# Kernel tuning notes

Measured on AMD Instinct MI355X. Metric: run time of the kernel, lower is better.

Reference implementation:

```python
import jax, jax.numpy as jnp
import numpy as np

B, L = 64, 2048
G, K, D = 16, 16, 256
N = G * K
STEPS = 32
MAX_NODES = 50
LN_EPS = 1e-5


def _gelu(x):
    return jax.nn.gelu(x, approximate=False)  # torch nn.GELU default = exact erf


def _mlp2(x, w1, b1, w2, b2):
    return _gelu(x @ w1 + b1) @ w2 + b2


def setup_inputs() -> dict:
    key = jax.random.key(0)
    ki = iter(jax.random.split(key, 64))
    def nrm(shape, s=0.02):
        return jax.random.normal(next(ki), shape, dtype=jnp.float32) * s
    inp = {}
    inp['src'] = jax.random.randint(next(ki), (B, L), 0, MAX_NODES)
    inp['rel'] = jax.random.randint(next(ki), (B, L), 0, 2)
    inp['tgt'] = jax.random.randint(next(ki), (B, L), 0, MAX_NODES)
    inp['mask'] = jnp.ones((B, L), dtype=bool)  # unused by forward, kept for signature parity
    inp['qsrc'] = jax.random.randint(next(ki), (B,), 0, MAX_NODES)
    inp['qtgt'] = jax.random.randint(next(ki), (B,), 0, MAX_NODES)
    inp['node_embed'] = nrm((MAX_NODES, D), 1.0)
    inp['rel_embed'] = nrm((2, D), 1.0)
    inp['edge_w1'] = nrm((3 * D, D)); inp['edge_b1'] = jnp.zeros((D,), jnp.float32)
    inp['edge_w2'] = nrm((D, D)); inp['edge_b2'] = jnp.zeros((D,), jnp.float32)
    inp['query_w1'] = nrm((2 * D, D)); inp['query_b1'] = jnp.zeros((D,), jnp.float32)
    inp['query_w2'] = nrm((D, D)); inp['query_b2'] = jnp.zeros((D,), jnp.float32)
    inp['gproj'] = nrm((D, G))
    inp['sproj'] = nrm((D, K))
    inp['msg_w1'] = nrm((D, 2 * D)); inp['msg_b1'] = jnp.zeros((2 * D,), jnp.float32)
    inp['msg_w2'] = nrm((2 * D, D)); inp['msg_b2'] = jnp.zeros((D,), jnp.float32)
    inp['gate_w1'] = nrm((D, D)); inp['gate_b1'] = jnp.zeros((D,), jnp.float32)
    inp['gate_w2'] = nrm((D, 1)); inp['gate_b2'] = jnp.zeros((1,), jnp.float32)
    inp['upd_w1'] = nrm((2 * D, 2 * D)); inp['upd_b1'] = jnp.zeros((2 * D,), jnp.float32)
    inp['upd_w2'] = nrm((2 * D, D)); inp['upd_b2'] = jnp.zeros((D,), jnp.float32)
    inp['ln_w'] = jnp.ones((D,), jnp.float32); inp['ln_b'] = jnp.zeros((D,), jnp.float32)
    inp['S_init'] = nrm((N, D))
    inp['head_w1'] = nrm((2 * D, D)); inp['head_b1'] = jnp.zeros((D,), jnp.float32)
    inp['head_w2'] = nrm((D, 2)); inp['head_b2'] = jnp.zeros((2,), jnp.float32)
    return inp


def _forward(src, rel, tgt, mask, qsrc, qtgt,
             node_embed, rel_embed,
             edge_w1, edge_b1, edge_w2, edge_b2,
             query_w1, query_b1, query_w2, query_b2,
             gproj, sproj,
             msg_w1, msg_b1, msg_w2, msg_b2,
             gate_w1, gate_b1, gate_w2, gate_b2,
             upd_w1, upd_b1, upd_w2, upd_b2,
             ln_w, ln_b, S_init,
             head_w1, head_b1, head_w2, head_b2):
    Bsz = src.shape[0]
    se = node_embed[jnp.clip(src, 0, MAX_NODES - 1)]          # (B, L, D)
    te = node_embed[jnp.clip(tgt, 0, MAX_NODES - 1)]
    re = rel_embed[rel]
    Xe = _mlp2(jnp.concatenate([se, re, te], -1), edge_w1, edge_b1, edge_w2, edge_b2)
    q = _mlp2(jnp.concatenate([node_embed[jnp.clip(qsrc, 0, MAX_NODES - 1)],
                               node_embed[jnp.clip(qtgt, 0, MAX_NODES - 1)]], -1),
              query_w1, query_b1, query_w2, query_b2)
    X = jnp.concatenate([Xe, q[:, None, :]], axis=1)          # (B, L+1, D)

    # Eval-mode hierarchical hard routing; X is constant across steps so the
    # message aggregation is loop-invariant and computed once (identical math).
    msg = _mlp2(X, msg_w1, msg_b1, msg_w2, msg_b2)
    gate = jax.nn.sigmoid(_mlp2(X, gate_w1, gate_b1, gate_w2, gate_b2))
    gated_msg = msg * gate                                    # (B, L+1, D)
    ga = jax.nn.one_hot(jnp.argmax(X @ gproj, axis=-1), G, dtype=X.dtype)  # (B,L+1,G)
    sa = jax.nn.one_hot(jnp.argmax(X @ sproj, axis=-1), K, dtype=X.dtype)  # (B,L+1,K)
    full_assign = (ga[..., :, None] * sa[..., None, :]).reshape(Bsz, X.shape[1], N)
    incoming = jnp.einsum('bln,bld->bnd', full_assign, gated_msg)          # (B, N, D)

    S0 = jnp.broadcast_to(S_init, (Bsz, N, D))

    def step(S, _):
        u = _mlp2(jnp.concatenate([S, incoming], -1), upd_w1, upd_b1, upd_w2, upd_b2)
        S = S + u
        mu = S.mean(-1, keepdims=True)
        var = ((S - mu) ** 2).mean(-1, keepdims=True)
        S = (S - mu) / jnp.sqrt(var + LN_EPS) * ln_w + ln_b
        return S, None

    S, _ = jax.lax.scan(step, S0, None, length=STEPS)
    bi = jnp.arange(Bsz)
    s_src = S[bi, jnp.clip(qsrc, 0, N - 1)]                   # (B, D)
    s_tgt = S[bi, jnp.clip(qtgt, 0, N - 1)]
    logits = _mlp2(jnp.concatenate([s_src, s_tgt], -1), head_w1, head_b1, head_w2, head_b2)
    return logits                                             # (B, 2)


def reference(src, rel, tgt, mask, qsrc, qtgt,
              node_embed, rel_embed,
              edge_w1, edge_b1, edge_w2, edge_b2,
              query_w1, query_b1, query_w2, query_b2,
              gproj, sproj,
              msg_w1, msg_b1, msg_w2, msg_b2,
              gate_w1, gate_b1, gate_w2, gate_b2,
              upd_w1, upd_b1, upd_w2, upd_b2,
              ln_w, ln_b, S_init,
              head_w1, head_b1, head_w2, head_b2):
    return _forward(src, rel, tgt, mask, qsrc, qtgt,
                    node_embed, rel_embed,
                    edge_w1, edge_b1, edge_w2, edge_b2,
                    query_w1, query_b1, query_w2, query_b2,
                    gproj, sproj,
                    msg_w1, msg_b1, msg_w2, msg_b2,
                    gate_w1, gate_b1, gate_w2, gate_b2,
                    upd_w1, upd_b1, upd_w2, upd_b2,
                    ln_w, ln_b, S_init,
                    head_w1, head_b1, head_w2, head_b2)
```

## Files before the change

### kernel.cpp

```cpp
#include <hip/hip_runtime.h>
#include <hip/hip_bf16.h>
#include <math.h>

#define NB     64
#define LL     2048
#define DD     256
#define NNODE  256
#define NSTEPS 32

typedef __hip_bfloat16 bf16;
typedef __attribute__((ext_vector_type(8))) short bf16x8;
typedef __attribute__((ext_vector_type(4))) float f32x4;

__device__ __forceinline__ float geluf(float x){ return 0.5f*x*(1.0f+erff(x*0.70710678118654752440f)); }
__device__ __forceinline__ short f2bs(float x){ bf16 h = __float2bfloat16(x); return __builtin_bit_cast(short, h); }
__device__ __forceinline__ float bs2f(short s){ bf16 h = __builtin_bit_cast(bf16, s); return __bfloat162float(h); }

__device__ __forceinline__ void split8(float4 a, float4 b, bf16x8& hi, bf16x8& lo){
  float av[8] = {a.x,a.y,a.z,a.w,b.x,b.y,b.z,b.w};
  #pragma unroll
  for(int j=0;j<8;j++){
    short h = f2bs(av[j]);
    hi[j] = h;
    lo[j] = f2bs(av[j] - bs2f(h));
  }
}
__device__ __forceinline__ bf16x8 cvt8(float4 a, float4 b){
  float av[8] = {a.x,a.y,a.z,a.w,b.x,b.y,b.z,b.w};
  bf16x8 v;
  #pragma unroll
  for(int j=0;j<8;j++) v[j] = f2bs(av[j]);
  return v;
}

__global__ __launch_bounds__(256) void k_precompute(const float* __restrict__ ne,
    const float* __restrict__ re, const float* __restrict__ ew1, const float* __restrict__ eb1,
    float* __restrict__ P){
  __shared__ float a[256];
  int row = blockIdx.x, j = threadIdx.x;
  const float* vec; const float* W;
  if(row < 50){ vec = ne + row*256; W = ew1; }
  else if(row < 52){ vec = re + (row-50)*256; W = ew1 + 256*256; }
  else { vec = ne + (row-52)*256; W = ew1 + 512*256; }
  a[j] = vec[j];
  __syncthreads();
  float acc = 0.f;
  for(int k=0;k<256;k++) acc += a[k]*W[k*256 + j];
  if(row >= 50 && row < 52) acc += eb1[j];
  P[row*256 + j] = acc;
}

__global__ __launch_bounds__(256) void k_query(const int* __restrict__ qsrc, const int* __restrict__ qtgt,
    const float* __restrict__ ne, const float* __restrict__ qw1, const float* __restrict__ qb1,
    const float* __restrict__ qw2, const float* __restrict__ qb2, float* __restrict__ qv){
  __shared__ float a[512];
  __shared__ float h[256];
  int b = blockIdx.x, j = threadIdx.x;
  int s = min(max(qsrc[b],0),49), t = min(max(qtgt[b],0),49);
  a[j]     = ne[s*256 + j];
  a[256+j] = ne[t*256 + j];
  __syncthreads();
  float acc = qb1[j];
  for(int k=0;k<512;k++) acc += a[k]*qw1[k*256+j];
  h[j] = geluf(acc);
  __syncthreads();
  float acc2 = qb2[j];
  for(int k=0;k<256;k++) acc2 += h[k]*qw2[k*256+j];
  qv[b*256+j] = acc2;
}

__global__ __launch_bounds__(256) void k_wprep(
    const float* __restrict__ uw1, const float* __restrict__ uw2,
    const float* __restrict__ ew2, const float* __restrict__ gw1,
    const float* __restrict__ mw1, const float* __restrict__ mw2,
    bf16* __restrict__ WTa, bf16* __restrict__ WT2,
    bf16* __restrict__ Weh, bf16* __restrict__ Wel, bf16* __restrict__ Wg,
    bf16* __restrict__ Wm1, bf16* __restrict__ Wm2){
  int i = blockIdx.x*256 + threadIdx.x;
  { int n = i >> 8, k = i & 255;  WTa[i] = __float2bfloat16(uw1[k*512 + n]); }
  { int n = i >> 9, k = i & 511;  WT2[i] = __float2bfloat16(uw2[k*256 + n]); }
  { int n = i >> 8, k = i & 255;  Wm1[i] = __float2bfloat16(mw1[k*512 + n]); }
  { int n = i >> 9, k = i & 511;  Wm2[i] = __float2bfloat16(mw2[k*256 + n]); }
  if(i < 65536){
    int n = i >> 8, k = i & 255;
    float v = ew2[k*256 + n];
    bf16 h = __float2bfloat16(v);
    Weh[i] = h;
    Wel[i] = __float2bfloat16(v - __bfloat162float(h));
    Wg[i]  = __float2bfloat16(gw1[k*256 + n]);
  }
}

#define AST 260
#define MST 520
__global__ __launch_bounds__(256,2) void k_edge_mfma(
    const int* __restrict__ src, const int* __restrict__ rel, const int* __restrict__ tgt,
    const float* __restrict__ P,
    const bf16* __restrict__ Weh, const bf16* __restrict__ Wel, const float* __restrict__ eb2,
    const bf16* __restrict__ Wg, const float* __restrict__ gb1,
    const float* __restrict__ gw2, const float* __restrict__ gb2,
    const float* __restrict__ gp, const float* __restrict__ sp,
    const bf16* __restrict__ Wm1, const float* __restrict__ mb1,
    const bf16* __restrict__ Wm2, const float* __restrict__ mb2,
    float* __restrict__ incoming)
{
  __shared__ __align__(16) float Af[32*AST];
  __shared__ __align__(16) float Xf[32*AST];
  __shared__ float pv[32*32];
  __shared__ float redG[32*4];
  __shared__ float gatev[32];
  __shared__ int   nidx[32];
  bf16* Mh = (bf16*)Af;

  int tid = threadIdx.x;
  int w = tid>>6, lane = tid&63, l15 = lane&15, l4 = lane>>4;
  int blk = blockIdx.x, b = blk>>6, r0 = (blk&63)*32;

  {
    int rr = tid&31, kb = (tid>>5)*32;
    int gr = b*LL + r0 + rr;
    int s = min(max(src[gr],0),49), rl = rel[gr]&1, t = min(max(tgt[gr],0),49);
    const float* ps = P + s*256;
    const float* pr = P + (50+rl)*256;
    const float* pt = P + (52+t)*256;
    #pragma unroll
    for(int j=0;j<32;j+=4){
      int k = kb+j;
      float4 vs = *(const float4*)(ps+k), vr = *(const float4*)(pr+k), vt = *(const float4*)(pt+k);
      float4 o;
      o.x = geluf(vs.x+vr.x+vt.x); o.y = geluf(vs.y+vr.y+vt.y);
      o.z = geluf(vs.z+vr.z+vt.z); o.w = geluf(vs.w+vr.w+vt.w);
      *(float4*)&Af[rr*AST + k] = o;
    }
  }
  __syncthreads();

  {
    f32x4 acc[2][4];
    #pragma unroll
    for(int mt=0;mt<2;mt++)
    #pragma unroll
    for(int nt=0;nt<4;nt++) acc[mt][nt] = (f32x4){0.f,0.f,0.f,0.f};
    for(int kc=0;kc<8;kc++){
      int k0 = kc*32 + l4*8;
      bf16x8 ah[2], al[2];
      #pragma unroll
      for(int mt=0;mt<2;mt++){
        const float* p = &Af[(mt*16+l15)*AST + k0];
        split8(*(const float4*)p, *(const float4*)(p+4), ah[mt], al[mt]);
      }
      #pragma unroll
      for(int nt=0;nt<4;nt++){
        int n = w*64 + nt*16 + l15;
        bf16x8 wh = *(const bf16x8*)&Weh[n*256 + k0];
        bf16x8 wl = *(const bf16x8*)&Wel[n*256 + k0];
        #pragma unroll
        for(int mt=0;mt<2;mt++){
          acc[mt][nt] = __builtin_amdgcn_mfma_f32_16x16x32_bf16(ah[mt], wh, acc[mt][nt], 0,0,0);
          acc[mt][nt] = __builtin_amdgcn_mfma_f32_16x16x32_bf16(ah[mt], wl, acc[mt][nt], 0,0,0);
          acc[mt][nt] = __builtin_amdgcn_mfma_f32_16x16x32_bf16(al[mt], wh, acc[mt][nt], 0,0,0);
        }
      }
    }
    #pragma unroll
    for(int nt=0;nt<4;nt++){
      int n = w*64 + nt*16 + l15;
      float bb = eb2[n];
      #pragma unroll
      for(int mt=0;mt<2;mt++)
      #pragma unroll
      for(int reg=0;reg<4;reg++){
        int r = mt*16 + l4*4 + reg;
        Xf[r*AST + n] = acc[mt][nt][reg] + bb;
      }
    }
  }
  __syncthreads();

  {
    f32x4 ag[2][4];
    #pragma unroll
    for(int mt=0;mt<2;mt++)
    #pragma unroll
    for(int nt=0;nt<4;nt++) ag[mt][nt] = (f32x4){0.f,0.f,0.f,0.f};
    for(int kc=0;kc<8;kc++){
      int k0 = kc*32 + l4*8;
      bf16x8 xa[2];
      #pragma unroll
      for(int mt=0;mt<2;mt++){
        const float* p = &Xf[(mt*16+l15)*AST + k0];
        xa[mt] = cvt8(*(const float4*)p, *(const float4*)(p+4));
      }
      #pragma unroll
      for(int nt=0;nt<4;nt++){
        int n = w*64 + nt*16 + l15;
        bf16x8 wv = *(const bf16x8*)&Wg[n*256 + k0];
        #pragma unroll
        for(int mt=0;mt<2;mt++)
          ag[mt][nt] = __builtin_amdgcn_mfma_f32_16x16x32_bf16(xa[mt], wv, ag[mt][nt], 0,0,0);
      }
    }
    float gpart[2][4] = {{0.f,0.f,0.f,0.f},{0.f,0.f,0.f,0.f}};
    #pragma unroll
    for(int nt=0;nt<4;nt++){
      int n = w*64 + nt*16 + l15;
      float gb = gb1[n], gw = gw2[n];
      #pragma unroll
      for(int mt=0;mt<2;mt++)
      #pragma unroll
      for(int reg=0;reg<4;reg++)
        gpart[mt][reg] += geluf(ag[mt][nt][reg] + gb)*gw;
    }
    #pragma unroll
    for(int mt=0;mt<2;mt++)
    #pragma unroll
    for(int reg=0;reg<4;reg++){
      float sv = gpart[mt][reg];
      #pragma unroll
      for(int o=1;o<16;o<<=1) sv += __shfl_xor(sv,o);
      if(l15==0) redG[(mt*16 + l4*4 + reg)*4 + w] = sv;
    }
  }
  {
    int r2 = tid>>3, g = tid&7, c0 = g*4;
    const float* W4 = (c0<16)? (gp + c0) : (sp + (c0-16));
    float4 p = {0.f,0.f,0.f,0.f};
    for(int k=0;k<256;k++){
      float x = Xf[r2*AST + k];
      float4 wv = *(const float4*)(W4 + k*16);
      p.x += x*wv.x; p.y += x*wv.y; p.z += x*wv.z; p.w += x*wv.w;
    }
    pv[r2*32+c0+0]=p.x; pv[r2*32+c0+1]=p.y; pv[r2*32+c0+2]=p.z; pv[r2*32+c0+3]=p.w;
  }
  __syncthreads();
  if(tid < 32){
    float ssum = redG[tid*4+0]+redG[tid*4+1]+redG[tid*4+2]+redG[tid*4+3] + gb2[0];
    gatev[tid] = 1.f/(1.f+expf(-ssum));
    float bg = pv[tid*32+0]; int big = 0;
    #pragma unroll
    for(int j=1;j<16;j++){ float x=pv[tid*32+j]; if(x>bg){bg=x;big=j;} }
    float bs = pv[tid*32+16]; int bis = 0;
    #pragma unroll
    for(int j=1;j<16;j++){ float x=pv[tid*32+16+j]; if(x>bs){bs=x;bis=j;} }
    nidx[tid] = big*16 + bis;
  }
  __syncthreads();

  {
    f32x4 a1[2][8];
    #pragma unroll
    for(int mt=0;mt<2;mt++)
    #pragma unroll
    for(int nt=0;nt<8;nt++) a1[mt][nt] = (f32x4){0.f,0.f,0.f,0.f};
    for(int kc=0;kc<8;kc++){
      int k0 = kc*32 + l4*8;
      bf16x8 xa[2];
      #pragma unroll
      for(int mt=0;mt<2;mt++){
        const float* p = &Xf[(mt*16+l15)*AST + k0];
        xa[mt] = cvt8(*(const float4*)p, *(const float4*)(p+4));
      }
      #pragma unroll
      for(int nt=0;nt<8;nt++){
        int n = w*128 + nt*16 + l15;
        bf16x8 wv = *(const bf16x8*)&Wm1[n*256 + k0];
        #pragma unroll
        for(int mt=0;mt<2;mt++)
          a1[mt][nt] = __builtin_amdgcn_mfma_f32_16x16x32_bf16(xa[mt], wv, a1[mt][nt], 0,0,0);
      }
    }
    __syncthreads();
    #pragma unroll
    for(int nt=0;nt<8;nt++){
      int n = w*128 + nt*16 + l15;
      float mb = mb1[n];
      #pragma unroll
      for(int mt=0;mt<2;mt++)
      #pragma unroll
      for(int reg=0;reg<4;reg++){
        int r = mt*16 + l4*4 + reg;
        Mh[r*MST + n] = __float2bfloat16(geluf(a1[mt][nt][reg] + mb));
      }
    }
  }
  __syncthreads();

  {
    f32x4 a2[2][4];
    #pragma unroll
    for(int mt=0;mt<2;mt++)
    #pragma unroll
    for(int nt=0;nt<4;nt++) a2[mt][nt] = (f32x4){0.f,0.f,0.f,0.f};
    for(int kc=0;kc<16;kc++){
      int k0 = kc*32 + l4*8;
      bf16x8 ha[2];
      #pragma unroll
      for(int mt=0;mt<2;mt++) ha[mt] = *(const bf16x8*)&Mh[(mt*16+l15)*MST + k0];
      #pragma unroll
      for(int nt=0;nt<4;nt++){
        int n = w*64 + nt*16 + l15;
        bf16x8 wv = *(const bf16x8*)&Wm2[n*512 + k0];
        #pragma unroll
        for(int mt=0;mt<2;mt++)
          a2[mt][nt] = __builtin_amdgcn_mfma_f32_16x16x32_bf16(ha[mt], wv, a2[mt][nt], 0,0,0);
      }
    }
    #pragma unroll
    for(int nt=0;nt<4;nt++){
      int col = w*64 + nt*16 + l15;
      float mb = mb2[col];
      #pragma unroll
      for(int mt=0;mt<2;mt++)
      #pragma unroll
      for(int reg=0;reg<4;reg++){
        int r = mt*16 + l4*4 + reg;
        float val = (a2[mt][nt][reg] + mb)*gatev[r];
        atomicAdd(&incoming[((size_t)b*NNODE + nidx[r])*256 + col], val);
      }
    }
  }
}

__global__ __launch_bounds__(256) void k_qrow(const float* __restrict__ qv,
    const float* __restrict__ mw1, const float* __restrict__ mb1,
    const float* __restrict__ mw2, const float* __restrict__ mb2,
    const float* __restrict__ gw1, const float* __restrict__ gb1,
    const float* __restrict__ gw2, const float* __restrict__ gb2,
    const float* __restrict__ gp, const float* __restrict__ sp,
    float* __restrict__ incoming){
  __shared__ float x[256];
  __shared__ float mh[512];
  __shared__ float gh[256];
  __shared__ float pv[32];
  __shared__ float rbuf[4];
  __shared__ float gv;
  __shared__ int nn;
  int b = blockIdx.x, j = threadIdx.x;
  x[j] = qv[b*256+j];
  __syncthreads();
  float a0 = mb1[j], a1 = mb1[256+j], g0 = gb1[j];
  for(int k=0;k<256;k++){
    float xv = x[k];
    a0 += xv*mw1[k*512+j];
    a1 += xv*mw1[k*512+256+j];
    g0 += xv*gw1[k*256+j];
  }
  mh[j] = geluf(a0); mh[256+j] = geluf(a1); gh[j] = geluf(g0);
  if(j < 32){
    float s1 = 0.f;
    const float* wq = (j<16)? gp+j : sp+(j-16);
    for(int k=0;k<256;k++) s1 += x[k]*wq[k*16];
    pv[j] = s1;
  }
  __syncthreads();
  float m0 = mb2[j];
  for(int k=0;k<512;k++) m0 += mh[k]*mw2[k*256+j];
  float part = gh[j]*gw2[j];
  for(int o=32;o>0;o>>=1) part += __shfl_down(part,o);
  if((j&63)==0) rbuf[j>>6] = part;
  __syncthreads();
  if(j==0){
    float s1 = rbuf[0]+rbuf[1]+rbuf[2]+rbuf[3];
    gv = 1.f/(1.f+expf(-(s1 + gb2[0])));
    float bg = pv[0]; int big = 0;
    for(int t2=1;t2<16;t2++){ if(pv[t2]>bg){bg=pv[t2];big=t2;} }
    float bs = pv[16]; int bis = 0;
    for(int t2=1;t2<16;t2++){ if(pv[16+t2]>bs){bs=pv[16+t2];bis=t2;} }
    nn = big*16 + bis;
  }
  __syncthreads();
  atomicAdd(&incoming[((size_t)b*NNODE + nn)*256 + j], m0*gv);
}

__device__ __forceinline__ void fma32_2q(const float* Arow, float w0, float w1, float* acc0, float* acc1){
  const float4* ap = (const float4*)Arow;
  #pragma unroll
  for(int i=0;i<8;i++){
    float4 a = ap[i];
    acc0[i*4+0] += a.x*w0; acc0[i*4+1] += a.y*w0;
    acc0[i*4+2] += a.z*w0; acc0[i*4+3] += a.w*w0;
    acc1[i*4+0] += a.x*w1; acc1[i*4+1] += a.y*w1;
    acc1[i*4+2] += a.z*w1; acc1[i*4+3] += a.w*w1;
  }
}
__global__ __launch_bounds__(256,2) void k_cpre(const float* __restrict__ incoming,
    const float* __restrict__ uw1, const float* __restrict__ ub1, float* __restrict__ Cpre){
  __shared__ float ATl[256*32];
  int blk = blockIdx.x, row0 = blk*32;
  int tid = threadIdx.x, rr = tid&31, kb = (tid>>5)*32;
  const float* ip = incoming + (size_t)(row0+rr)*256;
  #pragma unroll
  for(int j=0;j<32;j+=4){
    float4 v = *(const float4*)(ip+kb+j);
    ATl[(kb+j+0)*32+rr]=v.x; ATl[(kb+j+1)*32+rr]=v.y;
    ATl[(kb+j+2)*32+rr]=v.z; ATl[(kb+j+3)*32+rr]=v.w;
  }
  __syncthreads();
  float acc0[32], acc1[32];
  #pragma unroll
  for(int r=0;r<32;r++){acc0[r]=0.f;acc1[r]=0.f;}
  int c = tid;
  float w0 = uw1[256*512 + c], w1 = uw1[256*512 + 256 + c];
  for(int k=0;k<256;k++){
    float w0n = (k<255)? uw1[(257+k)*512 + c] : 0.f;
    float w1n = (k<255)? uw1[(257+k)*512 + 256 + c] : 0.f;
    fma32_2q(&ATl[k*32], w0, w1, acc0, acc1);
    w0 = w0n; w1 = w1n;
  }
  float b0 = ub1[c], b1 = ub1[256+c];
  #pragma unroll
  for(int r=0;r<32;r++){
    size_t ro = (size_t)(row0+r)*512;
    Cpre[ro+c]     = acc0[r]+b0;
    Cpre[ro+256+c] = acc1[r]+b1;
  }
}

#define SROW 264
#define HROW 520
__global__ __launch_bounds__(512,2) void k_steps(
    const float* __restrict__ Sini, const float* __restrict__ Cpre,
    const bf16* __restrict__ WTa, const bf16* __restrict__ WT2,
    const float* __restrict__ ub2, const float* __restrict__ lnw,
    const float* __restrict__ lnb, float* __restrict__ Sout)
{
  __shared__ __align__(16) bf16 Sbf[64*SROW];
  __shared__ __align__(16) bf16 Hbf[64*HROW];
  __shared__ float redA[64*8], redB[64*8];

  int tid = threadIdx.x;
  int w   = tid >> 6;
  int lane= tid & 63;
  int l15 = lane & 15;
  int l4  = lane >> 4;
  int row0 = blockIdx.x * 64;

  f32x4 Sreg[4][2];
  float ub[2], lw[2], lb[2];
  #pragma unroll
  for(int nt=0;nt<2;nt++){
    int col = w*32 + nt*16 + l15;
    ub[nt] = ub2[col]; lw[nt] = lnw[col]; lb[nt] = lnb[col];
  }
  #pragma unroll
  for(int mt=0;mt<4;mt++)
  #pragma unroll
  for(int nt=0;nt<2;nt++){
    int col = w*32 + nt*16 + l15;
    #pragma unroll
    for(int reg=0;reg<4;reg++){
      int r = mt*16 + l4*4 + reg;
      int node = (row0 + r) & 255;
      float v = Sini[node*256 + col];
      Sreg[mt][nt][reg] = v;
      Sbf[r*SROW + col] = __float2bfloat16(v);
    }
  }
  __syncthreads();

  const float* CpreBlk = Cpre + (size_t)row0*512;

  for(int step=0; step<NSTEPS; step++){
    f32x4 acc1[4][4];
    #pragma unroll
    for(int mt=0;mt<4;mt++)
    #pragma unroll
    for(int nt=0;nt<4;nt++) acc1[mt][nt] = (f32x4){0.f,0.f,0.f,0.f};
    const bf16* bp1[4];
    #pragma unroll
    for(int nt=0;nt<4;nt++) bp1[nt] = WTa + (size_t)(w*64 + nt*16 + l15)*256;
    for(int kc=0;kc<8;kc++){
      int k0 = kc*32 + l4*8;
      bf16x8 a[4];
      #pragma unroll
      for(int mt=0;mt<4;mt++) a[mt] = *(const bf16x8*)&Sbf[(mt*16 + l15)*SROW + k0];
      #pragma unroll
      for(int nt=0;nt<4;nt++){
        bf16x8 bfr = *(const bf16x8*)(bp1[nt] + k0);
        #pragma unroll
        for(int mt=0;mt<4;mt++)
          acc1[mt][nt] = __builtin_amdgcn_mfma_f32_16x16x32_bf16(a[mt], bfr, acc1[mt][nt], 0,0,0);
      }
    }
    #pragma unroll
    for(int nt=0;nt<4;nt++){
      int n = w*64 + nt*16 + l15;
      #pragma unroll
      for(int mt=0;mt<4;mt++)
      #pragma unroll
      for(int reg=0;reg<4;reg++){
        int r = mt*16 + l4*4 + reg;
        float cp = __builtin_nontemporal_load(&CpreBlk[(size_t)r*512 + n]);
        Hbf[r*HROW + n] = __float2bfloat16(geluf(acc1[mt][nt][reg] + cp));
      }
    }
    __syncthreads();

    f32x4 acc2[4][2];
    #pragma unroll
    for(int mt=0;mt<4;mt++)
    #pragma unroll
    for(int nt=0;nt<2;nt++) acc2[mt][nt] = (f32x4){0.f,0.f,0.f,0.f};
    const bf16* bp2[2];
    #pragma unroll
    for(int nt=0;nt<2;nt++) bp2[nt] = WT2 + (size_t)(w*32 + nt*16 + l15)*512;
    for(int kc=0;kc<16;kc++){
      int k0 = kc*32 + l4*8;
      bf16x8 a[4];
      #pragma unroll
      for(int mt=0;mt<4;mt++) a[mt] = *(const bf16x8*)&Hbf[(mt*16 + l15)*HROW + k0];
      #pragma unroll
      for(int nt=0;nt<2;nt++){
        bf16x8 bfr = *(const bf16x8*)(bp2[nt] + k0);
        #pragma unroll
        for(int mt=0;mt<4;mt++)
          acc2[mt][nt] = __builtin_amdgcn_mfma_f32_16x16x32_bf16(a[mt], bfr, acc2[mt][nt], 0,0,0);
      }
    }
    #pragma unroll
    for(int mt=0;mt<4;mt++)
    #pragma unroll
    for(int nt=0;nt<2;nt++)
    #pragma unroll
    for(int reg=0;reg<4;reg++)
      acc2[mt][nt][reg] = Sreg[mt][nt][reg] + acc2[mt][nt][reg] + ub[nt];

    #pragma unroll
    for(int mt=0;mt<4;mt++)
    #pragma unroll
    for(int reg=0;reg<4;reg++){
      float s1 = 0.f, s2 = 0.f;
      #pragma unroll
      for(int nt=0;nt<2;nt++){ float v = acc2[mt][nt][reg]; s1 += v; s2 += v*v; }
      #pragma unroll
      for(int o=1;o<16;o<<=1){ s1 += __shfl_xor(s1,o); s2 += __shfl_xor(s2,o); }
      if(l15 == 0){
        int r = mt*16 + l4*4 + reg;
        redA[r*8+w] = s1; redB[r*8+w] = s2;
      }
    }
    __syncthreads();

    #pragma unroll
    for(int mt=0;mt<4;mt++)
    #pragma unroll
    for(int reg=0;reg<4;reg++){
      int r = mt*16 + l4*4 + reg;
      float ss = 0.f, qq = 0.f;
      #pragma unroll
      for(int i=0;i<8;i++){ ss += redA[r*8+i]; qq += redB[r*8+i]; }
      float mu = ss*(1.f/256.f);
      float rs = rsqrtf(qq*(1.f/256.f) - mu*mu + 1e-5f);
      #pragma unroll
      for(int nt=0;nt<2;nt++){
        int col = w*32 + nt*16 + l15;
        float sv = (acc2[mt][nt][reg]-mu)*rs*lw[nt] + lb[nt];
        Sreg[mt][nt][reg] = sv;
        Sbf[r*SROW + col] = __float2bfloat16(sv);
      }
    }
    __syncthreads();
  }

  #pragma unroll
  for(int mt=0;mt<4;mt++)
  #pragma unroll
  for(int nt=0;nt<2;nt++){
    int col = w*32 + nt*16 + l15;
    #pragma unroll
    for(int reg=0;reg<4;reg++){
      int r = mt*16 + l4*4 + reg;
      Sout[(size_t)(row0+r)*256 + col] = Sreg[mt][nt][reg];
    }
  }
}

__global__ __launch_bounds__(256) void k_head(const int* __restrict__ qsrc, const int* __restrict__ qtgt,
    const float* __restrict__ S, const float* __restrict__ hw1, const float* __restrict__ hb1,
    const float* __restrict__ hw2, const float* __restrict__ hb2, float* __restrict__ out){
  __shared__ float a[512];
  __shared__ float h[256];
  __shared__ float rbuf[8];
  int b = blockIdx.x, j = threadIdx.x;
  int s = min(max(qsrc[b],0),255), t = min(max(qtgt[b],0),255);
  a[j]     = S[((size_t)b*NNODE + s)*256 + j];
  a[256+j] = S[((size_t)b*NNODE + t)*256 + j];
  __syncthreads();
  float acc = hb1[j];
  for(int k=0;k<512;k++) acc += a[k]*hw1[k*256+j];
  h[j] = geluf(acc);
  __syncthreads();
  float p0 = h[j]*hw2[j*2], p1 = h[j]*hw2[j*2+1];
  for(int o=32;o>0;o>>=1){ p0 += __shfl_down(p0,o); p1 += __shfl_down(p1,o); }
  if((j&63)==0){ rbuf[(j>>6)*2] = p0; rbuf[(j>>6)*2+1] = p1; }
  __syncthreads();
  if(j==0){
    out[b*2+0] = rbuf[0]+rbuf[2]+rbuf[4]+rbuf[6] + hb2[0];
    out[b*2+1] = rbuf[1]+rbuf[3]+rbuf[5]+rbuf[7] + hb2[1];
  }
}

extern "C" void kernel_launch(void* const* d_in, const int* in_sizes, int n_in,
                              void* d_out, int out_size, void* d_ws, size_t ws_size,
                              hipStream_t stream){
  (void)in_sizes; (void)n_in; (void)out_size; (void)ws_size;
  const int*  src  = (const int*)d_in[0];
  const int*  rel  = (const int*)d_in[1];
  const int*  tgt  = (const int*)d_in[2];
  const int*  qsrc = (const int*)d_in[4];
  const int*  qtgt = (const int*)d_in[5];
  const float* ne  = (const float*)d_in[6];
  const float* re  = (const float*)d_in[7];
  const float* ew1 = (const float*)d_in[8];  const float* eb1 = (const float*)d_in[9];
  const float* ew2 = (const float*)d_in[10]; const float* eb2 = (const float*)d_in[11];
  const float* qw1 = (const float*)d_in[12]; const float* qb1 = (const float*)d_in[13];
  const float* qw2 = (const float*)d_in[14]; const float* qb2 = (const float*)d_in[15];
  const float* gp  = (const float*)d_in[16]; const float* sp  = (const float*)d_in[17];
  const float* mw1 = (const float*)d_in[18]; const float* mb1 = (const float*)d_in[19];
  const float* mw2 = (const float*)d_in[20]; const float* mb2 = (const float*)d_in[21];
  const float* gw1 = (const float*)d_in[22]; const float* gb1 = (const float*)d_in[23];
  const float* gw2 = (const float*)d_in[24]; const float* gb2 = (const float*)d_in[25];
  const float* uw1 = (const float*)d_in[26]; const float* ub1 = (const float*)d_in[27];
  const float* uw2 = (const float*)d_in[28]; const float* ub2 = (const float*)d_in[29];
  const float* lnw = (const float*)d_in[30]; const float* lnb = (const float*)d_in[31];
  const float* Sini= (const float*)d_in[32];
  const float* hw1 = (const float*)d_in[33]; const float* hb1 = (const float*)d_in[34];
  const float* hw2 = (const float*)d_in[35]; const float* hb2 = (const float*)d_in[36];

  float* ws = (float*)d_ws;
  float* P        = ws;
  float* qv       = ws + 26112;
  float* incoming = ws + 42496;
  float* Cpre     = ws + 4236800;
  float* Sout     = ws + 12625408;
  bf16*  wb       = (bf16*)(ws + 16819712);
  bf16*  WTa = wb;            bf16* WT2 = wb + 131072;
  bf16*  Weh = wb + 262144;   bf16* Wel = wb + 327680;
  bf16*  Wg  = wb + 393216;
  bf16*  Wm1 = wb + 458752;   bf16* Wm2 = wb + 589824;
  float* out = (float*)d_out;

  hipMemsetAsync(incoming, 0, (size_t)4194304*4, stream);
  k_wprep<<<512,256,0,stream>>>(uw1,uw2,ew2,gw1,mw1,mw2,WTa,WT2,Weh,Wel,Wg,Wm1,Wm2);
  k_precompute<<<102,256,0,stream>>>(ne,re,ew1,eb1,P);
  k_query<<<64,256,0,stream>>>(qsrc,qtgt,ne,qw1,qb1,qw2,qb2,qv);
  k_edge_mfma<<<4096,256,0,stream>>>(src,rel,tgt,P,Weh,Wel,eb2,Wg,gb1,gw2,gb2,gp,sp,Wm1,mb1,Wm2,mb2,incoming);
  k_qrow<<<64,256,0,stream>>>(qv,mw1,mb1,mw2,mb2,gw1,gb1,gw2,gb2,gp,sp,incoming);
  k_cpre<<<512,256,0,stream>>>(incoming,uw1,ub1,Cpre);
  k_steps<<<256,512,0,stream>>>(Sini,Cpre,WTa,WT2,ub2,lnw,lnb,Sout);
  k_head<<<64,256,0,stream>>>(qsrc,qtgt,Sout,hw1,hb1,hw2,hb2,out);
}
```

Measured before the change: 3.327 ms.

## Register-cache Cpre across steps and software-prefetch weight fragments in GEMM loops

Loads the loop-invariant Cpre block into registers once before the 32-step recurrence, so it is no longer re-read from global memory every step. Both inner GEMM k-loops now double-buffer the global weight fragment, issuing next-iteration B loads before the current MFMAs to hide latency, and hoist the weight pointers out of the step loop. In exchange it uses 64 extra VGPRs for Creg plus prefetch buffers, which may reduce occupancy or cause spills.

Result: faster. 2.930 ms (-11.9%).

```diff
diff --git a/kernel.cpp b/kernel.cpp
--- a/kernel.cpp
+++ b/kernel.cpp
@@ -456,9 +456,28 @@
       Sbf[r*SROW + col] = __float2bfloat16(v);
     }
   }
-  __syncthreads();
 
   const float* CpreBlk = Cpre + (size_t)row0*512;
+  f32x4 Creg[4][4];
+  #pragma unroll
+  for(int nt=0;nt<4;nt++){
+    int n = w*64 + nt*16 + l15;
+    #pragma unroll
+    for(int mt=0;mt<4;mt++)
+    #pragma unroll
+    for(int reg=0;reg<4;reg++){
+      int r = mt*16 + l4*4 + reg;
+      Creg[mt][nt][reg] = CpreBlk[(size_t)r*512 + n];
+    }
+  }
+  __syncthreads();
+
+  const bf16* bp1[4];
+  #pragma unroll
+  for(int nt=0;nt<4;nt++) bp1[nt] = WTa + (size_t)(w*64 + nt*16 + l15)*256 + l4*8;
+  const bf16* bp2[2];
+  #pragma unroll
+  for(int nt=0;nt<2;nt++) bp2[nt] = WT2 + (size_t)(w*32 + nt*16 + l15)*512 + l4*8;
 
   for(int step=0; step<NSTEPS; step++){
     f32x4 acc1[4][4];
@@ -466,21 +485,25 @@
     for(int mt=0;mt<4;mt++)
     #pragma unroll
     for(int nt=0;nt<4;nt++) acc1[mt][nt] = (f32x4){0.f,0.f,0.f,0.f};
-    const bf16* bp1[4];
-    #pragma unroll
-    for(int nt=0;nt<4;nt++) bp1[nt] = WTa + (size_t)(w*64 + nt*16 + l15)*256;
+    bf16x8 b1c[4], b1n[4];
+    #pragma unroll
+    for(int nt=0;nt<4;nt++) b1c[nt] = *(const bf16x8*)(bp1[nt]);
     for(int kc=0;kc<8;kc++){
+      if(kc<7){
+        #pragma unroll
+        for(int nt=0;nt<4;nt++) b1n[nt] = *(const bf16x8*)(bp1[nt] + (kc+1)*32);
+      }
       int k0 = kc*32 + l4*8;
       bf16x8 a[4];
       #pragma unroll
       for(int mt=0;mt<4;mt++) a[mt] = *(const bf16x8*)&Sbf[(mt*16 + l15)*SROW + k0];
       #pragma unroll
-      for(int nt=0;nt<4;nt++){
-        bf16x8 bfr = *(const bf16x8*)(bp1[nt] + k0);
-        #pragma unroll
-        for(int mt=0;mt<4;mt++)
-          acc1[mt][nt] = __builtin_amdgcn_mfma_f32_16x16x32_bf16(a[mt], bfr, acc1[mt][nt], 0,0,0);
-      }
+      for(int nt=0;nt<4;nt++)
+      #pragma unroll
+      for(int mt=0;mt<4;mt++)
+        acc1[mt][nt] = __builtin_amdgcn_mfma_f32_16x16x32_bf16(a[mt], b1c[nt], acc1[mt][nt], 0,0,0);
+      #pragma unroll
+      for(int nt=0;nt<4;nt++) b1c[nt] = b1n[nt];
     }
     #pragma unroll
     for(int nt=0;nt<4;nt++){
@@ -490,8 +513,7 @@
       #pragma unroll
       for(int reg=0;reg<4;reg++){
         int r = mt*16 + l4*4 + reg;
-        float cp = __builtin_nontemporal_load(&CpreBlk[(size_t)r*512 + n]);
-        Hbf[r*HROW + n] = __float2bfloat16(geluf(acc1[mt][nt][reg] + cp));
+        Hbf[r*HROW + n] = __float2bfloat16(geluf(acc1[mt][nt][reg] + Creg[mt][nt][reg]));
       }
     }
     __syncthreads();
@@ -501,21 +523,25 @@
     for(int mt=0;mt<4;mt++)
     #pragma unroll
     for(int nt=0;nt<2;nt++) acc2[mt][nt] = (f32x4){0.f,0.f,0.f,0.f};
-    const bf16* bp2[2];
-    #pragma unroll
-    for(int nt=0;nt<2;nt++) bp2[nt] = WT2 + (size_t)(w*32 + nt*16 + l15)*512;
+    bf16x8 b2c[2], b2n[2];
+    #pragma unroll
+    for(int nt=0;nt<2;nt++) b2c[nt] = *(const bf16x8*)(bp2[nt]);
     for(int kc=0;kc<16;kc++){
+      if(kc<15){
+        #pragma unroll
+        for(int nt=0;nt<2;nt++) b2n[nt] = *(const bf16x8*)(bp2[nt] + (kc+1)*32);
+      }
       int k0 = kc*32 + l4*8;
       bf16x8 a[4];
       #pragma unroll
       for(int mt=0;mt<4;mt++) a[mt] = *(const bf16x8*)&Hbf[(mt*16 + l15)*HROW + k0];
       #pragma unroll
-      for(int nt=0;nt<2;nt++){
-        bf16x8 bfr = *(const bf16x8*)(bp2[nt] + k0);
-        #pragma unroll
-        for(int mt=0;mt<4;mt++)
-          acc2[mt][nt] = __builtin_amdgcn_mfma_f32_16x16x32_bf16(a[mt], bfr, acc2[mt][nt], 0,0,0);
-      }
+      for(int nt=0;nt<2;nt++)
+      #pragma unroll
+      for(int mt=0;mt<4;mt++)
+        acc2[mt][nt] = __builtin_amdgcn_mfma_f32_16x16x32_bf16(a[mt], b2c[nt], acc2[mt][nt], 0,0,0);
+      #pragma unroll
+      for(int nt=0;nt<2;nt++) b2c[nt] = b2n[nt];
     }
     #pragma unroll
     for(int mt=0;mt<4;mt++)
```
